# Kernel tuning notes

Hardware: AMD Instinct MI355X
Metric: run time of the kernel (lower is better)

The kernel has to match this reference:

```python
import jax, jax.numpy as jnp
import numpy as np

N_SHARD = 4
PPP = 512            # positive_per_partition
NEG = 1024           # padded_negative
E = 256              # embedding size
N_ENT = 250000       # entities per shard (local table)
N_REL = 1000


def setup_inputs() -> dict:
    key = jax.random.key(0)
    k1, k2, k3, k4, k5, k6 = jax.random.split(key, 6)
    return {
        "head": jax.random.randint(k1, (N_SHARD, PPP), 0, N_ENT),
        "relation": jax.random.randint(k2, (N_SHARD, PPP), 0, N_REL),
        "tail": jax.random.randint(k3, (N_SHARD, PPP), 0, N_ENT),
        "negative": jax.random.randint(k4, (N_SHARD, 1, NEG), 0, N_ENT),
        "entity_embedding": jax.random.normal(k5, (N_ENT, E), dtype=jnp.float32),
        "relation_embedding": jax.random.normal(k6, (N_REL, E), dtype=jnp.float32),
    }


def reference(head, relation, tail, negative, entity_embedding, relation_embedding):
    n_shard, ppp = head.shape
    emb_size = entity_embedding.shape[-1]

    # --- phase 1: gather local embeddings (single fused gather, as in the module) ---
    negative_flat = negative.reshape(n_shard, -1)                       # (S, NEG)
    gather_idx = jnp.concatenate([head, tail, negative_flat], axis=1)   # (S, 2*ppp+NEG)
    emb = entity_embedding[gather_idx]                                  # (S, 2*ppp+NEG, E)
    head_embedding = emb[:, :ppp]                                       # (S, ppp, E)
    tail_embedding = emb[:, ppp:2 * ppp]                                # (S, ppp, E)
    negative_embedding = emb[:, 2 * ppp:].reshape(*negative.shape, emb_size)  # (S,1,NEG,E)
    # flat negative format: single shared negative set
    negative_embedding = negative_embedding[0][None]                    # (1, 1, NEG, E)

    # --- phase 2: collectives (simulated on replicated data) ---
    # all_gather -> new leading n_shard dim
    relation_all = jnp.broadcast_to(relation, (n_shard, n_shard, ppp))  # (S, S, ppp)
    # corruption scheme 't': all_gather head embeddings
    head_embedding_all = jnp.broadcast_to(
        head_embedding, (n_shard, n_shard, ppp, emb_size))              # (S, S, ppp, E)

    # --- phase 3: scoring (DistMult, negative sample sharing) ---
    h = head_embedding_all.reshape(-1, emb_size)                        # (S*S*ppp, E)
    r = relation_embedding[relation_all.reshape(-1)]                    # (S*S*ppp, E)
    t_neg = negative_embedding.reshape(-1, emb_size)                    # (NEG, E)
    negative_score = jnp.einsum('ne,me->nm', h * r, t_neg)             # (S*S*ppp, NEG)

    # route scores back: reshape -> all_to_all (identity on replicated data)
    # -> transpose -> flatten, exactly as in the module
    negative_score = negative_score.reshape(n_shard, n_shard * ppp, -1)
    negative_score = jnp.transpose(negative_score, (1, 0, 2)).reshape(n_shard * ppp, -1)
    # (S*ppp, S*NEG)

    # tail_embedding = all_to_all(tail_embedding) -> identity in simulation
    hp = head_embedding.reshape(-1, emb_size)
    rp = relation_embedding[relation.reshape(-1)]
    tp = tail_embedding.reshape(-1, emb_size)
    positive_score = jnp.sum(hp * rp * tp, axis=-1)                     # (S*ppp,)

    return positive_score, negative_score
```

## Files before the change

kernel.cpp:

```cpp
#include <hip/hip_runtime.h>
#include <hip/hip_bf16.h>

#define N_SHARD 4
#define PPP     512
#define NEG_N   1024
#define EMB     256
#define NROWS   (N_SHARD * PPP)

typedef __attribute__((ext_vector_type(8))) short bf16x8;
typedef __attribute__((ext_vector_type(4))) float f32x4;

__device__ __forceinline__ unsigned short f2bf(float f) {
    union { float f; unsigned int u; } v; v.f = f;
    return (unsigned short)((v.u + 0x7FFFu + ((v.u >> 16) & 1u)) >> 16);
}

__device__ __forceinline__ void load16_to_lds(const void* g, void* l) {
    __builtin_amdgcn_global_load_lds(
        (const __attribute__((address_space(1))) unsigned int*)g,
        (__attribute__((address_space(3))) unsigned int*)l, 16, 0, 0);
}

__global__ __launch_bounds__(256) void prep_kernel(
    const int* __restrict__ head, const int* __restrict__ relation,
    const int* __restrict__ tail, const int* __restrict__ negative,
    const float* __restrict__ ent, const float* __restrict__ relemb,
    float* __restrict__ pos_out,
    unsigned short* __restrict__ hr_bf, unsigned short* __restrict__ t_bf)
{
    const int wave = blockIdx.x * 4 + (threadIdx.x >> 6);
    const int lane = threadIdx.x & 63;
    if (wave < NROWS) {
        const int n = wave;
        const int hi = head[n], ri = relation[n], ti = tail[n];
        const float4 h4 = ((const float4*)(ent    + (size_t)hi * EMB))[lane];
        const float4 r4 = ((const float4*)(relemb + (size_t)ri * EMB))[lane];
        const float4 t4 = ((const float4*)(ent    + (size_t)ti * EMB))[lane];
        const float x = h4.x * r4.x, y = h4.y * r4.y;
        const float z = h4.z * r4.z, w = h4.w * r4.w;
        const ushort4 s = make_ushort4(f2bf(x), f2bf(y), f2bf(z), f2bf(w));
        const int byte_in_row = (lane * 8) ^ ((n & 7) << 4);
        *(ushort4*)((char*)hr_bf + (size_t)n * 512 + byte_in_row) = s;
        float p = x * t4.x + y * t4.y + z * t4.z + w * t4.w;
        #pragma unroll
        for (int off = 32; off > 0; off >>= 1) p += __shfl_down(p, off, 64);
        if (lane == 0) pos_out[n] = p;
    } else if (wave < NROWS + NEG_N) {
        const int m = wave - NROWS;
        const int idx = negative[m];
        const float4 t4 = ((const float4*)(ent + (size_t)idx * EMB))[lane];
        const ushort4 s = make_ushort4(f2bf(t4.x), f2bf(t4.y), f2bf(t4.z), f2bf(t4.w));
        const int byte_in_row = (lane * 8) ^ ((m & 7) << 4);
        *(ushort4*)((char*)t_bf + (size_t)m * 512 + byte_in_row) = s;
    }
}

__global__ __launch_bounds__(256, 2) void gemm_kernel(
    const unsigned short* __restrict__ hr_bf,
    const unsigned short* __restrict__ t_bf,
    float* __restrict__ neg_out)
{
    __shared__ unsigned short Abuf[64 * EMB];
    __shared__ unsigned short Bbuf[64 * EMB];

    const int wid  = threadIdx.x >> 6;
    const int lane = threadIdx.x & 63;
    const int row_tile = blockIdx.x * 64;
    const int col_tile = blockIdx.y * 64;

    const char* aSrc = (const char*)(hr_bf + (size_t)row_tile * EMB);
    const char* bSrc = (const char*)(t_bf  + (size_t)col_tile * EMB);
    #pragma unroll
    for (int c = 0; c < 8; ++c) {
        const int chunk = (wid * 8 + c) * 1024;
        const int goff  = chunk + lane * 16;
        load16_to_lds(aSrc + goff, (char*)Abuf + chunk);
        load16_to_lds(bSrc + goff, (char*)Bbuf + chunk);
    }
    __syncthreads();

    const int r16  = lane & 15;
    const int half = lane >> 4;
    const int arow = wid * 16 + r16;
    const int aswz = (arow & 7) << 4;
    const int bswz = (r16 & 7) << 4;

    f32x4 acc0 = {0.f, 0.f, 0.f, 0.f};
    f32x4 acc1 = acc0, acc2 = acc0, acc3 = acc0;
    #pragma unroll
    for (int kk = 0; kk < 8; ++kk) {
        const int koff = kk * 64 + half * 16;
        const bf16x8 a  = *(const bf16x8*)((const char*)Abuf + arow * 512 + (koff ^ aswz));
        const bf16x8 b0 = *(const bf16x8*)((const char*)Bbuf + (r16 +  0) * 512 + (koff ^ bswz));
        const bf16x8 b1 = *(const bf16x8*)((const char*)Bbuf + (r16 + 16) * 512 + (koff ^ bswz));
        const bf16x8 b2 = *(const bf16x8*)((const char*)Bbuf + (r16 + 32) * 512 + (koff ^ bswz));
        const bf16x8 b3 = *(const bf16x8*)((const char*)Bbuf + (r16 + 48) * 512 + (koff ^ bswz));
        acc0 = __builtin_amdgcn_mfma_f32_16x16x32_bf16(a, b0, acc0, 0, 0, 0);
        acc1 = __builtin_amdgcn_mfma_f32_16x16x32_bf16(a, b1, acc1, 0, 0, 0);
        acc2 = __builtin_amdgcn_mfma_f32_16x16x32_bf16(a, b2, acc2, 0, 0, 0);
        acc3 = __builtin_amdgcn_mfma_f32_16x16x32_bf16(a, b3, acc3, 0, 0, 0);
    }

    float* cw = (float*)((char*)Abuf + wid * 8192);
    #pragma unroll
    for (int v = 0; v < 4; ++v) {
        const int lr = half * 4 + v;
        const float vals[4] = {acc0[v], acc1[v], acc2[v], acc3[v]};
        #pragma unroll
        for (int nf = 0; nf < 4; ++nf) {
            const int c = nf * 16 + r16;
            cw[lr * 64 + (c ^ (half << 4))] = vals[nf];
        }
    }
    #pragma unroll
    for (int j = 0; j < 4; ++j) {
        const int lr = j * 4 + half;
        const f32x4 v4 = *(const f32x4*)&cw[lr * 64 + ((r16 * 4) ^ (j << 4))];
        const int grow = row_tile + wid * 16 + lr;
        float* orow = neg_out + (size_t)grow * 4096 + col_tile + r16 * 4;
        __builtin_nontemporal_store(v4, (f32x4*)(orow));
        __builtin_nontemporal_store(v4, (f32x4*)(orow + 1024));
        __builtin_nontemporal_store(v4, (f32x4*)(orow + 2048));
        __builtin_nontemporal_store(v4, (f32x4*)(orow + 3072));
    }
}

extern "C" void kernel_launch(void* const* d_in, const int* in_sizes, int n_in,
                              void* d_out, int out_size, void* d_ws, size_t ws_size,
                              hipStream_t stream) {
    const int*   head     = (const int*)d_in[0];
    const int*   relation = (const int*)d_in[1];
    const int*   tail     = (const int*)d_in[2];
    const int*   negative = (const int*)d_in[3];
    const float* ent      = (const float*)d_in[4];
    const float* rel      = (const float*)d_in[5];

    float* pos_out = (float*)d_out;
    float* neg_out = (float*)d_out + NROWS;

    unsigned short* hr_bf = (unsigned short*)d_ws;
    unsigned short* t_bf  = hr_bf + (size_t)NROWS * EMB;

    prep_kernel<<<768, 256, 0, stream>>>(head, relation, tail, negative, ent, rel,
                                         pos_out, hr_bf, t_bf);
    gemm_kernel<<<dim3(32, 16), 256, 0, stream>>>(hr_bf, t_bf, neg_out);
}
```

Baseline: 19.21 us.

## Enlarge GEMM block tile to 64x128 and coarsen prep kernel work per wave

The GEMM kernel now runs 512-thread blocks that each compute a 64x128 output tile over a 1D grid of 256 blocks. This halves the number of times the A tile is loaded from global memory and makes the B tile reused by two wave columns. The prep kernel launches 256 blocks and each wave handles two positive rows plus one negative row, which removes the branchy tail blocks. The trade-off is fewer, larger blocks that may underfill the many CUs on the device, and a larger LDS footprint per block.

```diff
diff --git a/kernel.cpp b/kernel.cpp
--- a/kernel.cpp
+++ b/kernel.cpp
@@ -28,10 +28,13 @@
     float* __restrict__ pos_out,
     unsigned short* __restrict__ hr_bf, unsigned short* __restrict__ t_bf)
 {
-    const int wave = blockIdx.x * 4 + (threadIdx.x >> 6);
+    const int wid  = threadIdx.x >> 6;
     const int lane = threadIdx.x & 63;
-    if (wave < NROWS) {
-        const int n = wave;
+    const int gw   = blockIdx.x * 4 + wid;
+
+    #pragma unroll
+    for (int rep = 0; rep < 2; ++rep) {
+        const int n = gw + rep * 1024;
         const int hi = head[n], ri = relation[n], ti = tail[n];
         const float4 h4 = ((const float4*)(ent    + (size_t)hi * EMB))[lane];
         const float4 r4 = ((const float4*)(relemb + (size_t)ri * EMB))[lane];
@@ -45,8 +48,9 @@
         #pragma unroll
         for (int off = 32; off > 0; off >>= 1) p += __shfl_down(p, off, 64);
         if (lane == 0) pos_out[n] = p;
-    } else if (wave < NROWS + NEG_N) {
-        const int m = wave - NROWS;
+    }
+    {
+        const int m = gw;
         const int idx = negative[m];
         const float4 t4 = ((const float4*)(ent + (size_t)idx * EMB))[lane];
         const ushort4 s = make_ushort4(f2bf(t4.x), f2bf(t4.y), f2bf(t4.z), f2bf(t4.w));
@@ -55,69 +59,73 @@
     }
 }
 
-__global__ __launch_bounds__(256, 2) void gemm_kernel(
+__global__ __launch_bounds__(512, 1) void gemm_kernel(
     const unsigned short* __restrict__ hr_bf,
     const unsigned short* __restrict__ t_bf,
     float* __restrict__ neg_out)
 {
     __shared__ unsigned short Abuf[64 * EMB];
-    __shared__ unsigned short Bbuf[64 * EMB];
+    __shared__ unsigned short Bbuf[128 * EMB];
 
     const int wid  = threadIdx.x >> 6;
     const int lane = threadIdx.x & 63;
-    const int row_tile = blockIdx.x * 64;
-    const int col_tile = blockIdx.y * 64;
+    const int row0 = (blockIdx.x & 31) * 64;
+    const int col0 = (blockIdx.x >> 5) * 128;
 
-    const char* aSrc = (const char*)(hr_bf + (size_t)row_tile * EMB);
-    const char* bSrc = (const char*)(t_bf  + (size_t)col_tile * EMB);
+    const char* aSrc = (const char*)(hr_bf + (size_t)row0 * EMB);
+    const char* bSrc = (const char*)(t_bf  + (size_t)col0 * EMB);
+    #pragma unroll
+    for (int c = 0; c < 4; ++c) {
+        const int chunk = (wid * 4 + c) * 1024;
+        load16_to_lds(aSrc + chunk + lane * 16, (char*)Abuf + chunk);
+    }
     #pragma unroll
     for (int c = 0; c < 8; ++c) {
         const int chunk = (wid * 8 + c) * 1024;
-        const int goff  = chunk + lane * 16;
-        load16_to_lds(aSrc + goff, (char*)Abuf + chunk);
-        load16_to_lds(bSrc + goff, (char*)Bbuf + chunk);
+        load16_to_lds(bSrc + chunk + lane * 16, (char*)Bbuf + chunk);
     }
     __syncthreads();
 
     const int r16  = lane & 15;
     const int half = lane >> 4;
-    const int arow = wid * 16 + r16;
+    const int wr   = wid >> 1, wc = wid & 1;
+    const int arow = wr * 16 + r16;
     const int aswz = (arow & 7) << 4;
+    const int bb   = wc * 64;
     const int bswz = (r16 & 7) << 4;
 
-    f32x4 acc0 = {0.f, 0.f, 0.f, 0.f};
-    f32x4 acc1 = acc0, acc2 = acc0, acc3 = acc0;
+    f32x4 acc[4];
+    #pragma unroll
+    for (int nf = 0; nf < 4; ++nf) acc[nf] = (f32x4){0.f, 0.f, 0.f, 0.f};
+
     #pragma unroll
     for (int kk = 0; kk < 8; ++kk) {
         const int koff = kk * 64 + half * 16;
-        const bf16x8 a  = *(const bf16x8*)((const char*)Abuf + arow * 512 + (koff ^ aswz));
-        const bf16x8 b0 = *(const bf16x8*)((const char*)Bbuf + (r16 +  0) * 512 + (koff ^ bswz));
-        const bf16x8 b1 = *(const bf16x8*)((const char*)Bbuf + (r16 + 16) * 512 + (koff ^ bswz));
-        const bf16x8 b2 = *(const bf16x8*)((const char*)Bbuf + (r16 + 32) * 512 + (koff ^ bswz));
-        const bf16x8 b3 = *(const bf16x8*)((const char*)Bbuf + (r16 + 48) * 512 + (koff ^ bswz));
-        acc0 = __builtin_amdgcn_mfma_f32_16x16x32_bf16(a, b0, acc0, 0, 0, 0);
-        acc1 = __builtin_amdgcn_mfma_f32_16x16x32_bf16(a, b1, acc1, 0, 0, 0);
-        acc2 = __builtin_amdgcn_mfma_f32_16x16x32_bf16(a, b2, acc2, 0, 0, 0);
-        acc3 = __builtin_amdgcn_mfma_f32_16x16x32_bf16(a, b3, acc3, 0, 0, 0);
+        const bf16x8 a = *(const bf16x8*)((const char*)Abuf + arow * 512 + (koff ^ aswz));
+        #pragma unroll
+        for (int nf = 0; nf < 4; ++nf) {
+            const bf16x8 b = *(const bf16x8*)((const char*)Bbuf + (bb + nf * 16 + r16) * 512 + (koff ^ bswz));
+            acc[nf] = __builtin_amdgcn_mfma_f32_16x16x32_bf16(a, b, acc[nf], 0, 0, 0);
+        }
     }
+    __syncthreads();
 
-    float* cw = (float*)((char*)Abuf + wid * 8192);
+    float* cw = (float*)((char*)Abuf + wid * 4096);
     #pragma unroll
     for (int v = 0; v < 4; ++v) {
         const int lr = half * 4 + v;
-        const float vals[4] = {acc0[v], acc1[v], acc2[v], acc3[v]};
         #pragma unroll
         for (int nf = 0; nf < 4; ++nf) {
             const int c = nf * 16 + r16;
-            cw[lr * 64 + (c ^ (half << 4))] = vals[nf];
+            cw[lr * 64 + (c ^ (half << 4))] = acc[nf][v];
         }
     }
     #pragma unroll
     for (int j = 0; j < 4; ++j) {
         const int lr = j * 4 + half;
         const f32x4 v4 = *(const f32x4*)&cw[lr * 64 + ((r16 * 4) ^ (j << 4))];
-        const int grow = row_tile + wid * 16 + lr;
-        float* orow = neg_out + (size_t)grow * 4096 + col_tile + r16 * 4;
+        const int grow = row0 + wr * 16 + lr;
+        float* orow = neg_out + (size_t)grow * 4096 + col0 + wc * 64 + r16 * 4;
         __builtin_nontemporal_store(v4, (f32x4*)(orow));
         __builtin_nontemporal_store(v4, (f32x4*)(orow + 1024));
         __builtin_nontemporal_store(v4, (f32x4*)(orow + 2048));
@@ -141,7 +149,7 @@
     unsigned short* hr_bf = (unsigned short*)d_ws;
     unsigned short* t_bf  = hr_bf + (size_t)NROWS * EMB;
 
-    prep_kernel<<<768, 256, 0, stream>>>(head, relation, tail, negative, ent, rel,
-                                         pos_out, hr_bf, t_bf);
-    gemm_kernel<<<dim3(32, 16), 256, 0, stream>>>(hr_bf, t_bf, neg_out);
+    prep_kernel<<<256, 256, 0, stream>>>(head, relation, tail, negative,
+                                         ent, rel, pos_out, hr_bf, t_bf);
+    gemm_kernel<<<256, 512, 0, stream>>>(hr_bf, t_bf, neg_out);
 }
```

Result: faster. 18.51 us (-3.6%).
